# Optimization experiments

Hardware: AMD Instinct MI355X
Metric: run time of the kernel (lower is better)

## Reference

```python
import jax, jax.numpy as jnp
import numpy as np

B, S, D = 4, 2048, 1024

def setup_inputs() -> dict:
    key = jax.random.key(0)
    k0, k1, k2, k3 = jax.random.split(key, 4)
    scale = 1.0 / np.sqrt(D)
    return {
        "x": jax.random.normal(k0, (B, S, D), dtype=jnp.float32),
        "Wq": jax.random.normal(k1, (D, D), dtype=jnp.float32) * scale,
        "Wk": jax.random.normal(k2, (D, D), dtype=jnp.float32) * scale,
        "Wv": jax.random.normal(k3, (D, D), dtype=jnp.float32) * scale,
    }

def reference(x, Wq, Wk, Wv):
    # x: [B,S,D]; Wq/Wk/Wv: [D_in, D_out] (equivalent to torch Linear weight transposed)
    q = jnp.einsum('bsd,de->bse', x, Wq)
    k = jnp.einsum('bsd,de->bse', x, Wk)
    v = jnp.einsum('bsd,de->bse', x, Wv)
    d_out = k.shape[-1]
    scores = jnp.einsum('bqe,bke->bqk', q, k)  # [B,S,S]
    S_ = scores.shape[-1]
    causal = jnp.tril(jnp.ones((S_, S_), dtype=bool))  # True = keep
    # masked_fill before scaling == after scaling (-inf invariant under positive scale)
    scores = jnp.where(causal, scores, -jnp.inf)
    attn = jax.nn.softmax(scores / jnp.sqrt(jnp.asarray(d_out, scores.dtype)), axis=-1)
    # dropout p=0.0 -> identity
    return jnp.einsum('bqk,bke->bqe', attn, v)
```

## Files before the change

### kernel.cpp

```cpp
#include <hip/hip_runtime.h>

#define B_  4
#define S_  2048
#define D_  1024
#define N_  (B_*S_)
#define SCALE 0.03125f
#define NEGINF (-3.0e38f)

typedef unsigned short u16;
typedef __attribute__((ext_vector_type(8))) short short8;
typedef __attribute__((ext_vector_type(4))) float floatx4;

__device__ __forceinline__ u16 f2bf(float f) {
    unsigned int u = __float_as_uint(f);
    u += 0x7FFFu + ((u >> 16) & 1u);
    return (u16)(u >> 16);
}
__device__ __forceinline__ float bf2f(u16 h) {
    return __uint_as_float((unsigned int)h << 16);
}

__device__ __forceinline__ void gl_lds16(const void* g, void* l) {
    __builtin_amdgcn_global_load_lds(
        (const __attribute__((address_space(1))) unsigned int*)g,
        (__attribute__((address_space(3))) unsigned int*)l, 16, 0, 0);
}

__global__ __launch_bounds__(256) void cast_fused(const float* __restrict__ x,
                                                  const float* __restrict__ Wq, const float* __restrict__ Wk,
                                                  const float* __restrict__ Wv,
                                                  u16* __restrict__ xb, u16* __restrict__ Wqb,
                                                  u16* __restrict__ Wkb, u16* __restrict__ Wvt) {
    __shared__ float t[32][33];
    const int blk = blockIdx.x;
    if (blk < 5120) {
        const float* src; u16* dst; size_t i;
        if (blk < 4096)      { src = x;  dst = xb;  i = (size_t)blk * 2048; }
        else if (blk < 4608) { src = Wq; dst = Wqb; i = (size_t)(blk - 4096) * 2048; }
        else                 { src = Wk; dst = Wkb; i = (size_t)(blk - 4608) * 2048; }
        i += (size_t)threadIdx.x * 8;
        float4 a = *(const float4*)&src[i];
        float4 b = *(const float4*)&src[i + 4];
        short8 o;
        o[0]=f2bf(a.x); o[1]=f2bf(a.y); o[2]=f2bf(a.z); o[3]=f2bf(a.w);
        o[4]=f2bf(b.x); o[5]=f2bf(b.y); o[6]=f2bf(b.z); o[7]=f2bf(b.w);
        *(short8*)&dst[i] = o;
    } else {
        const int tb = blk - 5120;
        const int c = threadIdx.x & 31, r0 = threadIdx.x >> 5;
        const int i0 = (tb >> 5) * 32, j0 = (tb & 31) * 32;
#pragma unroll
        for (int rr = 0; rr < 4; ++rr)
            t[r0 + rr * 8][c] = Wv[(size_t)(i0 + r0 + rr * 8) * D_ + j0 + c];
        __syncthreads();
#pragma unroll
        for (int rr = 0; rr < 4; ++rr)
            Wvt[(size_t)(j0 + r0 + rr * 8) * D_ + i0 + c] = f2bf(t[c][r0 + rr * 8]);
    }
}

__device__ __forceinline__ void mfma_nt_loop(const u16* __restrict__ A, int lda,
                                             const u16* __restrict__ Bp, int ldb,
                                             int m0, int n0, int kext,
                                             u16* As, u16* Bs, floatx4 acc[4][4])
{
    const int tid  = threadIdx.x;
    const int lane = tid & 63;
    const int lr   = lane & 15, quad = lane >> 4;
    const int wm   = ((tid >> 6) & 1) * 64, wn = (tid >> 7) * 64;
    const int e    = tid * 8;
    const int nt   = kext >> 6;

    auto stage = [&](int k0, int half) {
        u16* Ad = As + half * 8192;
        u16* Bd = Bs + half * 8192;
#pragma unroll
        for (int it = 0; it < 4; ++it) {
            int idx = it * 2048 + e;
            int row = idx >> 6;
            int cg  = (idx & 63) >> 3;
            int gc  = (cg ^ (row & 7)) << 3;
            gl_lds16(&A [(size_t)(m0 + row) * lda + k0 + gc], &Ad[idx]);
            gl_lds16(&Bp[(size_t)(n0 + row) * ldb + k0 + gc], &Bd[idx]);
        }
    };

    stage(0, 0);
    int cur = 0;
    for (int t = 0; t < nt; ++t) {
        if (t + 1 < nt) {
            stage((t + 1) << 6, cur ^ 1);
            asm volatile("s_waitcnt vmcnt(8)" ::: "memory");
        } else {
            asm volatile("s_waitcnt vmcnt(0)" ::: "memory");
        }
        __builtin_amdgcn_s_barrier();

        const u16* Asb = As + cur * 8192;
        const u16* Bsb = Bs + cur * 8192;
#pragma unroll
        for (int kk = 0; kk < 2; ++kk) {
            short8 af[4], bf[4];
            const int kg = kk * 4 + quad;
#pragma unroll
            for (int i = 0; i < 4; ++i) {
                int am = wm + i * 16 + lr;
                af[i] = *(const short8*)&Asb[am * 64 + ((kg ^ (am & 7)) << 3)];
                int bn = wn + i * 16 + lr;
                bf[i] = *(const short8*)&Bsb[bn * 64 + ((kg ^ (bn & 7)) << 3)];
            }
            __builtin_amdgcn_s_setprio(1);
#pragma unroll
            for (int i = 0; i < 4; ++i)
#pragma unroll
                for (int j = 0; j < 4; ++j)
                    acc[i][j] = __builtin_amdgcn_mfma_f32_16x16x32_bf16(af[i], bf[j], acc[i][j], 0, 0, 0);
            __builtin_amdgcn_s_setprio(0);
        }
        asm volatile("s_waitcnt lgkmcnt(0)" ::: "memory");
        __builtin_amdgcn_s_barrier();
        cur ^= 1;
    }
}

#define EPI_VARS                                              \
    const int lane = threadIdx.x & 63;                        \
    const int lr = lane & 15, quad = lane >> 4;               \
    const int wm = ((threadIdx.x >> 6) & 1) * 64, wn = (threadIdx.x >> 7) * 64;

__global__ __launch_bounds__(256) void mt_mfma(const u16* __restrict__ Wkb, const u16* __restrict__ Wqb,
                                               u16* __restrict__ Mt)
{
    __shared__ u16 As[16384], Bs[16384];
    const int m0 = blockIdx.y * 128, n0 = blockIdx.x * 128;
    floatx4 acc[4][4];
#pragma unroll
    for (int i = 0; i < 4; ++i)
#pragma unroll
        for (int j = 0; j < 4; ++j) acc[i][j] = (floatx4){0.f, 0.f, 0.f, 0.f};
    mfma_nt_loop(Wkb, D_, Wqb, D_, m0, n0, D_, As, Bs, acc);

    EPI_VARS
#pragma unroll
    for (int i = 0; i < 4; ++i)
#pragma unroll
        for (int j = 0; j < 4; ++j)
#pragma unroll
            for (int r = 0; r < 4; ++r)
                Mt[(size_t)(m0 + wm + i * 16 + quad * 4 + r) * D_ + n0 + wn + j * 16 + lr] = f2bf(acc[i][j][r]);
}

__global__ __launch_bounds__(256) void yv_mfma(const u16* __restrict__ xb, const u16* __restrict__ Mt,
                                               const u16* __restrict__ Wvt,
                                               u16* __restrict__ Y, u16* __restrict__ Vt)
{
    __shared__ u16 As[16384], Bs[16384];
    const int id = blockIdx.x;
    floatx4 acc[4][4];
#pragma unroll
    for (int i = 0; i < 4; ++i)
#pragma unroll
        for (int j = 0; j < 4; ++j) acc[i][j] = (floatx4){0.f, 0.f, 0.f, 0.f};

    if (id < 512) {
        const int m0 = (id >> 3) * 128, n0 = (id & 7) * 128;
        mfma_nt_loop(xb, D_, Mt, D_, m0, n0, D_, As, Bs, acc);
        EPI_VARS
#pragma unroll
        for (int i = 0; i < 4; ++i)
#pragma unroll
            for (int j = 0; j < 4; ++j)
#pragma unroll
                for (int r = 0; r < 4; ++r)
                    Y[(size_t)(m0 + wm + i * 16 + quad * 4 + r) * D_ + n0 + wn + j * 16 + lr] = f2bf(acc[i][j][r]);
    } else {
        const int v = id - 512;
        const int b = v >> 7;
        const int mloc = ((v >> 3) & 15) * 128;
        const int n0 = (v & 7) * 128;
        const int m0 = b * S_ + mloc;
        u16* Vb = Vt + (size_t)b * D_ * S_;
        mfma_nt_loop(xb, D_, Wvt, D_, m0, n0, D_, As, Bs, acc);
        EPI_VARS
#pragma unroll
        for (int i = 0; i < 4; ++i)
#pragma unroll
            for (int j = 0; j < 4; ++j) {
                const int ee = n0 + wn + j * 16 + lr;
                const int s4 = mloc + wm + i * 16 + quad * 4;
                ushort4 o;
                o.x = f2bf(acc[i][j][0]); o.y = f2bf(acc[i][j][1]);
                o.z = f2bf(acc[i][j][2]); o.w = f2bf(acc[i][j][3]);
                *(ushort4*)&Vb[(size_t)ee * S_ + s4] = o;
            }
    }
}

__global__ __launch_bounds__(256) void scores_mfma(const u16* __restrict__ Y, const u16* __restrict__ xb,
                                                   u16* __restrict__ Sc)
{
    const int t = blockIdx.x, b = blockIdx.z;
    int qt = (int)((sqrtf(8.0f * t + 1.0f) - 1.0f) * 0.5f);
    while ((qt + 1) * (qt + 2) / 2 <= t) ++qt;
    while (qt * (qt + 1) / 2 > t) --qt;
    const int kt = t - qt * (qt + 1) / 2;

    __shared__ u16 As[16384], Bs[16384];
    const u16* A  = Y  + (size_t)b * S_ * D_;
    const u16* Bp = xb + (size_t)b * S_ * D_;
    u16* Sb = Sc + (size_t)b * S_ * S_;
    const int m0 = qt * 128, n0 = kt * 128;
    floatx4 acc[4][4];
#pragma unroll
    for (int i = 0; i < 4; ++i)
#pragma unroll
        for (int j = 0; j < 4; ++j) acc[i][j] = (floatx4){0.f, 0.f, 0.f, 0.f};
    mfma_nt_loop(A, D_, Bp, D_, m0, n0, D_, As, Bs, acc);

    EPI_VARS
#pragma unroll
    for (int i = 0; i < 4; ++i)
#pragma unroll
        for (int r = 0; r < 4; ++r) {
            const int grow = m0 + wm + i * 16 + quad * 4 + r;
#pragma unroll
            for (int j = 0; j < 4; ++j) {
                const int gcol = n0 + wn + j * 16 + lr;
                const float v = (gcol <= grow) ? acc[i][j][r] * SCALE : NEGINF;
                Sb[(size_t)grow * S_ + gcol] = f2bf(v);
            }
        }
}

__global__ __launch_bounds__(256) void softmax_k(const u16* __restrict__ Sc, u16* __restrict__ P)
{
    const int row = blockIdx.x;
    const int b = row >> 11, q = row & (S_ - 1);
    const int L = ((q >> 7) + 1) << 7;
    const u16* rp = Sc + ((size_t)b * S_ + q) * S_;
    u16* pp = P + ((size_t)b * S_ + q) * S_;
    __shared__ float red[4];
    __shared__ float bc;
    const int tid = threadIdx.x;
    const int i = tid << 3;
    const bool act = i < L;

    float f[8];
    float lmax = -3.4e38f;
    if (act) {
        short8 v = *(const short8*)&rp[i];
#pragma unroll
        for (int k = 0; k < 8; ++k) { f[k] = bf2f((u16)v[k]); lmax = fmaxf(lmax, f[k]); }
    }
    for (int off = 32; off; off >>= 1) lmax = fmaxf(lmax, __shfl_down(lmax, off, 64));
    if ((tid & 63) == 0) red[tid >> 6] = lmax;
    __syncthreads();
    if (tid == 0) bc = fmaxf(fmaxf(red[0], red[1]), fmaxf(red[2], red[3]));
    __syncthreads();
    const float m = bc;

    float lsum = 0.f;
    if (act) {
#pragma unroll
        for (int k = 0; k < 8; ++k) { f[k] = __expf(f[k] - m); lsum += f[k]; }
    }
    for (int off = 32; off; off >>= 1) lsum += __shfl_down(lsum, off, 64);
    if ((tid & 63) == 0) red[tid >> 6] = lsum;
    __syncthreads();
    if (tid == 0) bc = red[0] + red[1] + red[2] + red[3];
    __syncthreads();
    const float inv = 1.0f / bc;

    if (act) {
        short8 o;
#pragma unroll
        for (int k = 0; k < 8; ++k) o[k] = (short)f2bf(f[k] * inv);
        *(short8*)&pp[i] = o;
    }
}

__global__ __launch_bounds__(256) void pv_mfma(const u16* __restrict__ P, const u16* __restrict__ Vt,
                                               float* __restrict__ O)
{
    const int et = blockIdx.x, qt = blockIdx.y, b = blockIdx.z;
    __shared__ u16 As[16384], Bs[16384];
    const u16* A  = P  + (size_t)b * S_ * S_;
    const u16* Bp = Vt + (size_t)b * D_ * S_;
    const int m0 = qt * 128, n0 = et * 128;
    const int kext = (qt + 1) * 128;
    floatx4 acc[4][4];
#pragma unroll
    for (int i = 0; i < 4; ++i)
#pragma unroll
        for (int j = 0; j < 4; ++j) acc[i][j] = (floatx4){0.f, 0.f, 0.f, 0.f};
    mfma_nt_loop(A, S_, Bp, S_, m0, n0, kext, As, Bs, acc);

    EPI_VARS
#pragma unroll
    for (int i = 0; i < 4; ++i)
#pragma unroll
        for (int r = 0; r < 4; ++r) {
            const int grow = m0 + wm + i * 16 + quad * 4 + r;
#pragma unroll
            for (int j = 0; j < 4; ++j)
                O[((size_t)b * S_ + grow) * D_ + n0 + wn + j * 16 + lr] = acc[i][j][r];
        }
}

extern "C" void kernel_launch(void* const* d_in, const int* in_sizes, int n_in,
                              void* d_out, int out_size, void* d_ws, size_t ws_size,
                              hipStream_t stream) {
    const float* x  = (const float*)d_in[0];
    const float* Wq = (const float*)d_in[1];
    const float* Wk = (const float*)d_in[2];
    const float* Wv = (const float*)d_in[3];
    float* out = (float*)d_out;
    char* w = (char*)d_ws;

    u16* xb  = (u16*)(w);
    u16* Wqb = (u16*)(w + 16777216);
    u16* Wkb = (u16*)(w + 18874368);
    u16* Wvt = (u16*)(w + 20971520);
    u16* Mt  = (u16*)(w + 23068672);
    u16* Y   = (u16*)(w + 25165824);
    u16* Vt  = (u16*)(w + 41943040);
    u16* Sc  = (u16*)(w + 58720256);
    u16* P   = (u16*)(w + 92274688);

    cast_fused <<<dim3(6144),        256, 0, stream>>>(x, Wq, Wk, Wv, xb, Wqb, Wkb, Wvt);
    mt_mfma    <<<dim3(8, 8),        256, 0, stream>>>(Wkb, Wqb, Mt);
    yv_mfma    <<<dim3(1024),        256, 0, stream>>>(xb, Mt, Wvt, Y, Vt);
    scores_mfma<<<dim3(136, 1, B_),  256, 0, stream>>>(Y, xb, Sc);
    softmax_k  <<<dim3(N_),          256, 0, stream>>>(Sc, P);
    pv_mfma    <<<dim3(8, 16, B_),   256, 0, stream>>>(P, Vt, out);
}
```

Measured before the change: 249.3 us.

## Use 256x256 tiles with 8-wave blocks for projection and score GEMMs, XCD-swizzle blocks

Adds a 512-thread GEMM mainloop that computes 256x256 output tiles and double-buffers 64-wide K slices in 128KB of LDS. Four stage/compute phases per K step split the next slice's loads across them. The Y/V projection and causal score kernels move to this mainloop to raise arithmetic intensity and cut global and LDS traffic per FLOP. Block indices in these kernels and in the PV kernel are remapped so neighbouring tiles share an XCD's L2. The trade-off is fewer, larger blocks (144 for scores, 256 for projections), which can leave CUs idle and wastes more work on masked diagonal tiles.

New measurement: 233.9 us. -6.2%, faster.

```diff
diff --git a/kernel.cpp b/kernel.cpp
--- a/kernel.cpp
+++ b/kernel.cpp
@@ -24,6 +24,10 @@
     __builtin_amdgcn_global_load_lds(
         (const __attribute__((address_space(1))) unsigned int*)g,
         (__attribute__((address_space(3))) unsigned int*)l, 16, 0, 0);
+}
+
+__device__ __forceinline__ int xcd_chunk(int bid, int nwg) {
+    return (bid & 7) * (nwg >> 3) + (bid >> 3);
 }
 
 __global__ __launch_bounds__(256) void cast_fused(const float* __restrict__ x,
@@ -128,6 +132,109 @@
     const int lr = lane & 15, quad = lane >> 4;               \
     const int wm = ((threadIdx.x >> 6) & 1) * 64, wn = (threadIdx.x >> 7) * 64;
 
+__device__ __forceinline__ void mfma_nt_256(const u16* __restrict__ A, int lda,
+                                            const u16* __restrict__ Bp, int ldb,
+                                            int m0, int n0, int kext,
+                                            u16* As, u16* Bs, floatx4 acc[8][4])
+{
+    const int tid  = threadIdx.x;
+    const int lane = tid & 63;
+    const int lr   = lane & 15, quad = lane >> 4;
+    const int wid  = tid >> 6;
+    const int wr   = wid >> 2;
+    const int wc   = wid & 3;
+    const int nt   = kext >> 6;
+
+    auto stage2 = [&](int t, int c0) {
+        const int k0 = t << 6;
+        u16* Ad = As + (t & 1) * 16384;
+        u16* Bd = Bs + (t & 1) * 16384;
+#pragma unroll
+        for (int c = c0; c < c0 + 2; ++c) {
+            int idx = (c & 3) * 4096 + tid * 8;
+            int row = idx >> 6;
+            int cg  = (idx & 63) >> 3;
+            int gc  = (cg ^ (row & 7)) << 3;
+            if (c < 4) gl_lds16(&A [(size_t)(m0 + row) * lda + k0 + gc], &Ad[idx]);
+            else       gl_lds16(&Bp[(size_t)(n0 + row) * ldb + k0 + gc], &Bd[idx]);
+        }
+    };
+
+    stage2(0, 0); stage2(0, 2); stage2(0, 4); stage2(0, 6);
+
+    for (int t = 0; t < nt; ++t) {
+        const u16* Asb = As + (t & 1) * 16384;
+        const u16* Bsb = Bs + (t & 1) * 16384;
+        const bool pf = (t + 1 < nt);
+
+        short8 af[4][2], bfA[2][2], bfB[2][2];
+
+#pragma unroll
+        for (int p = 0; p < 4; ++p) {
+            if (p == 0) {
+                if (pf) { stage2(t + 1, 0);
+                          asm volatile("s_waitcnt vmcnt(2)" ::: "memory"); }
+                else      asm volatile("s_waitcnt vmcnt(0)" ::: "memory");
+                __builtin_amdgcn_s_barrier();
+            } else if (pf) {
+                stage2(t + 1, p * 2);
+            }
+
+            if (p == 0) {
+#pragma unroll
+                for (int i = 0; i < 4; ++i) {
+                    int am = wr * 128 + i * 16 + lr;
+#pragma unroll
+                    for (int kk = 0; kk < 2; ++kk)
+                        af[i][kk] = *(const short8*)&Asb[am * 64 + (((kk * 4 + quad) ^ (am & 7)) << 3)];
+                }
+#pragma unroll
+                for (int j = 0; j < 2; ++j) {
+                    int bn = wc * 64 + j * 16 + lr;
+#pragma unroll
+                    for (int kk = 0; kk < 2; ++kk)
+                        bfA[j][kk] = *(const short8*)&Bsb[bn * 64 + (((kk * 4 + quad) ^ (bn & 7)) << 3)];
+                }
+            } else if (p == 1) {
+#pragma unroll
+                for (int j = 0; j < 2; ++j) {
+                    int bn = wc * 64 + (j + 2) * 16 + lr;
+#pragma unroll
+                    for (int kk = 0; kk < 2; ++kk)
+                        bfB[j][kk] = *(const short8*)&Bsb[bn * 64 + (((kk * 4 + quad) ^ (bn & 7)) << 3)];
+                }
+            } else if (p == 2) {
+#pragma unroll
+                for (int i = 0; i < 4; ++i) {
+                    int am = wr * 128 + (i + 4) * 16 + lr;
+#pragma unroll
+                    for (int kk = 0; kk < 2; ++kk)
+                        af[i][kk] = *(const short8*)&Asb[am * 64 + (((kk * 4 + quad) ^ (am & 7)) << 3)];
+                }
+            }
+
+            const int mb = (p >> 1) * 4, nb = (p & 1) * 2;
+            __builtin_amdgcn_s_setprio(1);
+#pragma unroll
+            for (int kk = 0; kk < 2; ++kk)
+#pragma unroll
+                for (int i = 0; i < 4; ++i)
+#pragma unroll
+                    for (int j = 0; j < 2; ++j)
+                        acc[mb + i][nb + j] = __builtin_amdgcn_mfma_f32_16x16x32_bf16(
+                            af[i][kk], (p & 1) ? bfB[j][kk] : bfA[j][kk], acc[mb + i][nb + j], 0, 0, 0);
+            __builtin_amdgcn_s_setprio(0);
+            asm volatile("s_waitcnt lgkmcnt(0)" ::: "memory");
+            __builtin_amdgcn_s_barrier();
+        }
+    }
+}
+
+#define EPI256_VARS                                           \
+    const int lane = threadIdx.x & 63;                        \
+    const int lr = lane & 15, quad = lane >> 4;               \
+    const int wr = (threadIdx.x >> 8) & 1, wc = (threadIdx.x >> 6) & 3;
+
 __global__ __launch_bounds__(256) void mt_mfma(const u16* __restrict__ Wkb, const u16* __restrict__ Wqb,
                                                u16* __restrict__ Mt)
 {
@@ -150,44 +257,45 @@
                 Mt[(size_t)(m0 + wm + i * 16 + quad * 4 + r) * D_ + n0 + wn + j * 16 + lr] = f2bf(acc[i][j][r]);
 }
 
-__global__ __launch_bounds__(256) void yv_mfma(const u16* __restrict__ xb, const u16* __restrict__ Mt,
-                                               const u16* __restrict__ Wvt,
-                                               u16* __restrict__ Y, u16* __restrict__ Vt)
-{
-    __shared__ u16 As[16384], Bs[16384];
-    const int id = blockIdx.x;
-    floatx4 acc[4][4];
-#pragma unroll
-    for (int i = 0; i < 4; ++i)
+__global__ __launch_bounds__(512, 2) void yv_mfma(const u16* __restrict__ xb, const u16* __restrict__ Mt,
+                                                  const u16* __restrict__ Wvt,
+                                                  u16* __restrict__ Y, u16* __restrict__ Vt)
+{
+    __shared__ u16 As[32768], Bs[32768];
+    const int lid = xcd_chunk(blockIdx.x, 256);
+    floatx4 acc[8][4];
+#pragma unroll
+    for (int i = 0; i < 8; ++i)
 #pragma unroll
         for (int j = 0; j < 4; ++j) acc[i][j] = (floatx4){0.f, 0.f, 0.f, 0.f};
 
-    if (id < 512) {
-        const int m0 = (id >> 3) * 128, n0 = (id & 7) * 128;
-        mfma_nt_loop(xb, D_, Mt, D_, m0, n0, D_, As, Bs, acc);
-        EPI_VARS
-#pragma unroll
-        for (int i = 0; i < 4; ++i)
+    if (lid < 128) {
+        const int m0 = (lid >> 2) * 256, n0 = (lid & 3) * 256;
+        mfma_nt_256(xb, D_, Mt, D_, m0, n0, D_, As, Bs, acc);
+        EPI256_VARS
+#pragma unroll
+        for (int i = 0; i < 8; ++i)
 #pragma unroll
             for (int j = 0; j < 4; ++j)
 #pragma unroll
                 for (int r = 0; r < 4; ++r)
-                    Y[(size_t)(m0 + wm + i * 16 + quad * 4 + r) * D_ + n0 + wn + j * 16 + lr] = f2bf(acc[i][j][r]);
+                    Y[(size_t)(m0 + wr * 128 + i * 16 + quad * 4 + r) * D_ + n0 + wc * 64 + j * 16 + lr]
+                        = f2bf(acc[i][j][r]);
     } else {
-        const int v = id - 512;
-        const int b = v >> 7;
-        const int mloc = ((v >> 3) & 15) * 128;
-        const int n0 = (v & 7) * 128;
+        const int v = lid - 128;
+        const int b = v >> 5;
+        const int mloc = ((v >> 2) & 7) * 256;
+        const int n0 = (v & 3) * 256;
         const int m0 = b * S_ + mloc;
         u16* Vb = Vt + (size_t)b * D_ * S_;
-        mfma_nt_loop(xb, D_, Wvt, D_, m0, n0, D_, As, Bs, acc);
-        EPI_VARS
-#pragma unroll
-        for (int i = 0; i < 4; ++i)
+        mfma_nt_256(xb, D_, Wvt, D_, m0, n0, D_, As, Bs, acc);
+        EPI256_VARS
+#pragma unroll
+        for (int i = 0; i < 8; ++i)
 #pragma unroll
             for (int j = 0; j < 4; ++j) {
-                const int ee = n0 + wn + j * 16 + lr;
-                const int s4 = mloc + wm + i * 16 + quad * 4;
+                const int ee = n0 + wc * 64 + j * 16 + lr;
+                const int s4 = mloc + wr * 128 + i * 16 + quad * 4;
                 ushort4 o;
                 o.x = f2bf(acc[i][j][0]); o.y = f2bf(acc[i][j][1]);
                 o.z = f2bf(acc[i][j][2]); o.w = f2bf(acc[i][j][3]);
@@ -196,36 +304,37 @@
     }
 }
 
-__global__ __launch_bounds__(256) void scores_mfma(const u16* __restrict__ Y, const u16* __restrict__ xb,
-                                                   u16* __restrict__ Sc)
-{
-    const int t = blockIdx.x, b = blockIdx.z;
-    int qt = (int)((sqrtf(8.0f * t + 1.0f) - 1.0f) * 0.5f);
+__global__ __launch_bounds__(512, 2) void scores_mfma(const u16* __restrict__ Y, const u16* __restrict__ xb,
+                                                      u16* __restrict__ Sc)
+{
+    __shared__ u16 As[32768], Bs[32768];
+    const int lid = xcd_chunk(blockIdx.x, 144);
+    const int b = lid / 36;
+    const int t = lid - b * 36;
+    int qt = 0;
     while ((qt + 1) * (qt + 2) / 2 <= t) ++qt;
-    while (qt * (qt + 1) / 2 > t) --qt;
     const int kt = t - qt * (qt + 1) / 2;
 
-    __shared__ u16 As[16384], Bs[16384];
     const u16* A  = Y  + (size_t)b * S_ * D_;
     const u16* Bp = xb + (size_t)b * S_ * D_;
     u16* Sb = Sc + (size_t)b * S_ * S_;
-    const int m0 = qt * 128, n0 = kt * 128;
-    floatx4 acc[4][4];
-#pragma unroll
-    for (int i = 0; i < 4; ++i)
+    const int m0 = qt * 256, n0 = kt * 256;
+    floatx4 acc[8][4];
+#pragma unroll
+    for (int i = 0; i < 8; ++i)
 #pragma unroll
         for (int j = 0; j < 4; ++j) acc[i][j] = (floatx4){0.f, 0.f, 0.f, 0.f};
-    mfma_nt_loop(A, D_, Bp, D_, m0, n0, D_, As, Bs, acc);
-
-    EPI_VARS
-#pragma unroll
-    for (int i = 0; i < 4; ++i)
+    mfma_nt_256(A, D_, Bp, D_, m0, n0, D_, As, Bs, acc);
+
+    EPI256_VARS
+#pragma unroll
+    for (int i = 0; i < 8; ++i)
 #pragma unroll
         for (int r = 0; r < 4; ++r) {
-            const int grow = m0 + wm + i * 16 + quad * 4 + r;
+            const int grow = m0 + wr * 128 + i * 16 + quad * 4 + r;
 #pragma unroll
             for (int j = 0; j < 4; ++j) {
-                const int gcol = n0 + wn + j * 16 + lr;
+                const int gcol = n0 + wc * 64 + j * 16 + lr;
                 const float v = (gcol <= grow) ? acc[i][j][r] * SCALE : NEGINF;
                 Sb[(size_t)grow * S_ + gcol] = f2bf(v);
             }
@@ -282,7 +391,10 @@
 __global__ __launch_bounds__(256) void pv_mfma(const u16* __restrict__ P, const u16* __restrict__ Vt,
                                                float* __restrict__ O)
 {
-    const int et = blockIdx.x, qt = blockIdx.y, b = blockIdx.z;
+    const int lid = xcd_chunk(blockIdx.x, 512);
+    const int b  = lid >> 7;
+    const int r  = lid & 127;
+    const int et = r >> 4, qt = r & 15;
     __shared__ u16 As[16384], Bs[16384];
     const u16* A  = P  + (size_t)b * S_ * S_;
     const u16* Bp = Vt + (size_t)b * D_ * S_;
@@ -299,11 +411,11 @@
 #pragma unroll
     for (int i = 0; i < 4; ++i)
 #pragma unroll
-        for (int r = 0; r < 4; ++r) {
-            const int grow = m0 + wm + i * 16 + quad * 4 + r;
+        for (int r2 = 0; r2 < 4; ++r2) {
+            const int grow = m0 + wm + i * 16 + quad * 4 + r2;
 #pragma unroll
             for (int j = 0; j < 4; ++j)
-                O[((size_t)b * S_ + grow) * D_ + n0 + wn + j * 16 + lr] = acc[i][j][r];
+                O[((size_t)b * S_ + grow) * D_ + n0 + wn + j * 16 + lr] = acc[i][j][r2];
         }
 }
 
@@ -327,10 +439,10 @@
     u16* Sc  = (u16*)(w + 58720256);
     u16* P   = (u16*)(w + 92274688);
 
-    cast_fused <<<dim3(6144),        256, 0, stream>>>(x, Wq, Wk, Wv, xb, Wqb, Wkb, Wvt);
-    mt_mfma    <<<dim3(8, 8),        256, 0, stream>>>(Wkb, Wqb, Mt);
-    yv_mfma    <<<dim3(1024),        256, 0, stream>>>(xb, Mt, Wvt, Y, Vt);
-    scores_mfma<<<dim3(136, 1, B_),  256, 0, stream>>>(Y, xb, Sc);
-    softmax_k  <<<dim3(N_),          256, 0, stream>>>(Sc, P);
-    pv_mfma    <<<dim3(8, 16, B_),   256, 0, stream>>>(P, Vt, out);
-}
+    cast_fused <<<dim3(6144),   256, 0, stream>>>(x, Wq, Wk, Wv, xb, Wqb, Wkb, Wvt);
+    mt_mfma    <<<dim3(8, 8),   256, 0, stream>>>(Wkb, Wqb, Mt);
+    yv_mfma    <<<dim3(256),    512, 0, stream>>>(xb, Mt, Wvt, Y, Vt);
+    scores_mfma<<<dim3(144),    512, 0, stream>>>(Y, xb, Sc);
+    softmax_k  <<<dim3(N_),     256, 0, stream>>>(Sc, P);
+    pv_mfma    <<<dim3(512),    256, 0, stream>>>(P, Vt, out);
+}
```
